# Kernel optimization log

Measured on AMD Instinct MI355X. Metric: run time of the kernel, lower is better.

Reference implementation:

```python
import jax, jax.numpy as jnp
import numpy as np

B, N, D, E, R = 2, 50000, 128, 500000, 500
LN_EPS = 1e-5


def setup_inputs() -> dict:
    key = jax.random.key(0)
    ks = jax.random.split(key, 12)
    s = 1.0 / np.sqrt(D)
    s2 = 1.0 / np.sqrt(2 * D)
    return {
        "h": jax.random.normal(ks[0], (B, N, D), dtype=jnp.float32),
        "edge_src": jax.random.randint(ks[1], (E,), 0, N),
        "edge_tgt": jax.random.randint(ks[2], (E,), 0, N),
        "edge_rel": jax.random.randint(ks[3], (E,), 0, R),
        "nE": N,
        "msg_W": jax.random.uniform(ks[4], (D, D), jnp.float32, -s, s),
        "rel_emb": jax.random.normal(ks[5], (R, D), dtype=jnp.float32),
        "gate_W": jax.random.uniform(ks[6], (D, D), jnp.float32, -s, s),
        "update_W": jax.random.uniform(ks[7], (2 * D, D), jnp.float32, -s2, s2),
        "update_b": jax.random.uniform(ks[8], (D,), jnp.float32, -s2, s2),
        "ln_gamma": jnp.ones((D,), jnp.float32),
        "ln_beta": jnp.zeros((D,), jnp.float32),
    }


def reference(h, edge_src, edge_tgt, edge_rel, nE, msg_W, rel_emb, gate_W,
              update_W, update_b, ln_gamma, ln_beta):
    r = rel_emb[edge_rel]                      # [E, D]
    h_src = h[:, edge_src]                     # [B, E, D] gather
    gate = jax.nn.sigmoid(h_src @ gate_W)      # [B, E, D]
    msg = (h_src @ msg_W) * r[None] * gate     # [B, E, D]
    # scatter_add over target nodes
    h_agg = jnp.zeros((h.shape[0], nE, h.shape[2]), h.dtype)
    h_agg = h_agg.at[:, edge_tgt].add(msg)     # [B, N, D]
    upd = jnp.concatenate([h, h_agg], axis=-1) @ update_W + update_b
    x = h + jax.nn.relu(upd)
    mu = jnp.mean(x, axis=-1, keepdims=True)
    var = jnp.var(x, axis=-1, keepdims=True)
    h_new = (x - mu) * jax.lax.rsqrt(var + LN_EPS) * ln_gamma + ln_beta
    return h_new
```

## Files before the change

### kernel.cpp

```cpp
#include <hip/hip_runtime.h>

#define DD 128
#define NN 50000
#define BB 2
#define EE 500000
#define CAP 64
#define LN_EPS 1e-5f

typedef __attribute__((ext_vector_type(8))) short bf16x8;
typedef __attribute__((ext_vector_type(4))) float f32x4;

union FragU { unsigned short u[8]; unsigned int q[4]; bf16x8 v; };

__device__ __forceinline__ unsigned short f2bf(float x) {
  union { float f; unsigned u; } v; v.f = x;
  unsigned r = (v.u + 0x7FFFu + ((v.u >> 16) & 1u)) >> 16;
  return (unsigned short)r;
}
__device__ __forceinline__ float bfbits(short s) {
  union { unsigned u; float f; } v;
  v.u = ((unsigned)(unsigned short)s) << 16;
  return v.f;
}
__device__ __forceinline__ float sigmoidf(float x) {
  return 1.0f / (1.0f + __expf(-x));
}

__device__ __forceinline__ void stage16(const void* g, void* l) {
  __builtin_amdgcn_global_load_lds(
      (const __attribute__((address_space(1))) unsigned int*)g,
      (__attribute__((address_space(3))) unsigned int*)l, 16, 0, 0);
}

__global__ __launch_bounds__(256) void k_node(
    const float* __restrict__ h, const float* __restrict__ gate_W,
    const float* __restrict__ msg_W, unsigned short* __restrict__ P,
    const float* __restrict__ rel_emb, unsigned short* __restrict__ relb,
    int* __restrict__ deg, int BN)
{
  __shared__ float Hs[3][2048];

  const int t    = threadIdx.x;

  {
    const int gid  = blockIdx.x * 256 + t;
    const int gsz2 = gridDim.x * 256;
    for (int i = gid; i < 500 * 64; i += gsz2) {
      const float a = rel_emb[2 * i];
      const float b = rel_emb[2 * i + 1];
      *(unsigned int*)&relb[2 * i] =
          (unsigned int)f2bf(a) | ((unsigned int)f2bf(b) << 16);
    }
    for (int i = gid; i < NN; i += gsz2) deg[i] = 0;
    asm volatile("s_waitcnt vmcnt(0)" ::: "memory");
    __builtin_amdgcn_sched_barrier(0);
  }

  const int lane = t & 63;
  const int n16  = lane & 15;
  const int quad = lane >> 4;
  const int wave = t >> 6;

  FragU ag[2][4], am[2][4];
#pragma unroll
  for (int fi = 0; fi < 2; fi++) {
    const int frow = (wave + fi * 4) * 16 + n16;
#pragma unroll
    for (int ks = 0; ks < 4; ks++) {
      const int k0 = ks * 32 + quad * 8;
#pragma unroll
      for (int e = 0; e < 8; e++) {
        ag[fi][ks].u[e] = f2bf(gate_W[(size_t)(k0 + e) * DD + frow]);
        am[fi][ks].u[e] = f2bf(msg_W[(size_t)(k0 + e) * DD + frow]);
      }
    }
  }

  const int sr = t >> 5, sc = t & 31;
  const size_t g0 = (size_t)sr * 512 +
                    (size_t)((((sc & 24) | ((sc & 7) ^ (sr & 7)))) << 4);

  const int nT    = BN >> 4;
  const int gstep = gridDim.x;
  const int bid   = blockIdx.x;
  const char* hB  = (const char*)h;

#define NSTAGE(slot, tl)                                                     \
  do {                                                                       \
    const char* gb = hB + ((size_t)(tl) << 13);                              \
    char* lb = (char*)&Hs[slot][0];                                          \
    stage16(gb + g0, lb + t * 16);                                           \
    stage16(gb + g0 + 4096, lb + 4096 + t * 16);                             \
  } while (0)

  if (bid < nT)         NSTAGE(0, bid);
  if (bid + gstep < nT) NSTAGE(1, bid + gstep);

  int s = 0;
  for (int tile = bid; tile < nT; tile += gstep) {
    asm volatile("s_waitcnt vmcnt(2)" ::: "memory");
    __builtin_amdgcn_s_barrier();
    asm volatile("" ::: "memory");
    __builtin_amdgcn_sched_barrier(0);

    const float* hs = &Hs[s][0];
    bf16x8 bfr[4];
#pragma unroll
    for (int ks = 0; ks < 4; ks++) {
      const int cc = ks * 8 + quad * 2;
      const int w0 = (cc & 24) | ((cc & 7) ^ (n16 & 7));
      const int w1 = ((cc + 1) & 24) | (((cc + 1) & 7) ^ (n16 & 7));
      const float4 x0 = *(const float4*)(hs + n16 * 128 + w0 * 4);
      const float4 x1 = *(const float4*)(hs + n16 * 128 + w1 * 4);
      FragU f;
      f.u[0] = f2bf(x0.x); f.u[1] = f2bf(x0.y);
      f.u[2] = f2bf(x0.z); f.u[3] = f2bf(x0.w);
      f.u[4] = f2bf(x1.x); f.u[5] = f2bf(x1.y);
      f.u[6] = f2bf(x1.z); f.u[7] = f2bf(x1.w);
      bfr[ks] = f.v;
    }

    f32x4 accg[2], accm[2];
#pragma unroll
    for (int fi = 0; fi < 2; fi++) { accg[fi] = (f32x4)0.f; accm[fi] = (f32x4)0.f; }

#pragma unroll
    for (int fi = 0; fi < 2; fi++)
#pragma unroll
      for (int ks = 0; ks < 4; ks++) {
        accg[fi] = __builtin_amdgcn_mfma_f32_16x16x32_bf16(ag[fi][ks].v, bfr[ks], accg[fi], 0, 0, 0);
        accm[fi] = __builtin_amdgcn_mfma_f32_16x16x32_bf16(am[fi][ks].v, bfr[ks], accm[fi], 0, 0, 0);
      }

    const int b    = (tile * 16 >= NN) ? 1 : 0;
    const int node = tile * 16 + n16 - b * NN;
    unsigned short* Pr = P + (size_t)node * 256 + b * 128;
#pragma unroll
    for (int fi = 0; fi < 2; fi++) {
      const int ft = wave + fi * 4;
      const float v0 = accm[fi][0] * sigmoidf(accg[fi][0]);
      const float v1 = accm[fi][1] * sigmoidf(accg[fi][1]);
      const float v2 = accm[fi][2] * sigmoidf(accg[fi][2]);
      const float v3 = accm[fi][3] * sigmoidf(accg[fi][3]);
      uint2 o;
      o.x = (unsigned int)f2bf(v0) | ((unsigned int)f2bf(v1) << 16);
      o.y = (unsigned int)f2bf(v2) | ((unsigned int)f2bf(v3) << 16);
      *(uint2*)(Pr + ft * 16 + quad * 4) = o;
    }

    asm volatile("" ::: "memory");
    if (tile + 2 * gstep < nT) {
      int s2 = s + 2; if (s2 >= 3) s2 -= 3;
      NSTAGE(s2, tile + 2 * gstep);
    }
    s = (s + 1 >= 3) ? 0 : s + 1;
  }
#undef NSTAGE
}

__global__ __launch_bounds__(256) void k_fill_direct(
    const int* __restrict__ esrc, const int* __restrict__ etgt,
    const int* __restrict__ erel, int* __restrict__ deg,
    int* __restrict__ packed)
{
  const int e = blockIdx.x * 256 + threadIdx.x;
  if (e < EE) {
    const int tgt = etgt[e];
    const int pos = atomicAdd(&deg[tgt], 1);
    if (pos < CAP) packed[(size_t)tgt * CAP + pos] = esrc[e] | (erel[e] << 16);
  }
}

__global__ __launch_bounds__(256) void k_agg(
    const unsigned short* __restrict__ P, const unsigned short* __restrict__ relb,
    const int* __restrict__ deg, const int* __restrict__ packed,
    unsigned short* __restrict__ h_agg)
{
  const int node = blockIdx.x * 4 + (threadIdx.x >> 6);
  if (node >= NN) return;
  const int lane = threadIdx.x & 63;
  const int half = lane >> 5;
  const int c8   = (lane & 31) * 8;
  const int rc   = c8 & 127;

  const int beg = node * CAP;
  const int cnt = min(deg[node], CAP);
  const int end = beg + cnt;

  float acc[8];
#pragma unroll
  for (int i = 0; i < 8; i++) acc[i] = 0.f;

  int j = beg + half;
  for (; j + 2 < end; j += 4) {
    const int p0 = packed[j];
    const int p1 = packed[j + 2];
    const bf16x8 pv0 = *(const bf16x8*)(P + (size_t)(p0 & 0xFFFF) * 256 + c8);
    const bf16x8 rv0 = *(const bf16x8*)(relb + (size_t)(p0 >> 16) * DD + rc);
    const bf16x8 pv1 = *(const bf16x8*)(P + (size_t)(p1 & 0xFFFF) * 256 + c8);
    const bf16x8 rv1 = *(const bf16x8*)(relb + (size_t)(p1 >> 16) * DD + rc);
#pragma unroll
    for (int i = 0; i < 8; i++) {
      acc[i] += bfbits(pv0[i]) * bfbits(rv0[i]);
      acc[i] += bfbits(pv1[i]) * bfbits(rv1[i]);
    }
  }
  for (; j < end; j += 2) {
    const int p0 = packed[j];
    const bf16x8 pv0 = *(const bf16x8*)(P + (size_t)(p0 & 0xFFFF) * 256 + c8);
    const bf16x8 rv0 = *(const bf16x8*)(relb + (size_t)(p0 >> 16) * DD + rc);
#pragma unroll
    for (int i = 0; i < 8; i++) acc[i] += bfbits(pv0[i]) * bfbits(rv0[i]);
  }

#pragma unroll
  for (int i = 0; i < 8; i++) acc[i] += __shfl_xor(acc[i], 32, 64);

  if (half == 0) {
    uint4 o;
    o.x = (unsigned int)f2bf(acc[0]) | ((unsigned int)f2bf(acc[1]) << 16);
    o.y = (unsigned int)f2bf(acc[2]) | ((unsigned int)f2bf(acc[3]) << 16);
    o.z = (unsigned int)f2bf(acc[4]) | ((unsigned int)f2bf(acc[5]) << 16);
    o.w = (unsigned int)f2bf(acc[6]) | ((unsigned int)f2bf(acc[7]) << 16);
    *(uint4*)(h_agg + (size_t)node * 256 + c8) = o;
  }
}

__global__ __launch_bounds__(256) void k_update_ln(
    const float* __restrict__ h, const unsigned short* __restrict__ h_agg,
    const float* __restrict__ upd_W, const float* __restrict__ upd_b,
    const float* __restrict__ gamma, const float* __restrict__ beta,
    float* __restrict__ out, int BN)
{
  __shared__ float Us[3][3072];
  __shared__ float Rs[4][16], Rq[4][16];

  const int t    = threadIdx.x;
  const int lane = t & 63;
  const int n16  = lane & 15;
  const int quad = lane >> 4;
  const int wave = t >> 6;

  FragU aw[2][8];
#pragma unroll
  for (int fi = 0; fi < 2; fi++) {
    const int frow = (wave + fi * 4) * 16 + n16;
#pragma unroll
    for (int ks = 0; ks < 8; ks++) {
      const int k0 = ks * 32 + quad * 8;
#pragma unroll
      for (int e = 0; e < 8; e++)
        aw[fi][ks].u[e] = f2bf(upd_W[(size_t)(k0 + e) * DD + frow]);
    }
  }

  float4 bv[2], gv[2], btv[2];
#pragma unroll
  for (int fi = 0; fi < 2; fi++) {
    const int f0 = (wave + fi * 4) * 16 + quad * 4;
    bv[fi]  = *(const float4*)(upd_b + f0);
    gv[fi]  = *(const float4*)(gamma + f0);
    btv[fi] = *(const float4*)(beta + f0);
  }

  const int sr = t >> 5, sc = t & 31;
  const size_t g0 = (size_t)sr * 512 +
                    (size_t)((((sc & 24) | ((sc & 7) ^ (sr & 7)))) << 4);
  const int ar = t >> 4, ac = t & 15;
  const size_t ga0 = (size_t)ar * 512 +
                     (size_t)((((ac & 8) | ((ac & 7) ^ (ar & 7)))) << 4);

  const int nT    = BN >> 4;
  const int gstep = gridDim.x;
  const int bid   = blockIdx.x;
  const char* hB  = (const char*)h;
  const char* aB  = (const char*)h_agg;

#define USTAGE(slot, tl)                                                     \
  do {                                                                       \
    const char* gb = hB + ((size_t)(tl) << 13);                              \
    char* lb = (char*)&Us[slot][0];                                          \
    stage16(gb + g0, lb + t * 16);                                           \
    stage16(gb + g0 + 4096, lb + 4096 + t * 16);                             \
    const int bb = ((tl) * 16 >= NN) ? 1 : 0;                                \
    const size_t node0 = (size_t)(tl) * 16 - (size_t)bb * NN;                \
    stage16(aB + (node0 << 9) + ((size_t)bb << 8) + ga0, lb + 8192 + t * 16);\
  } while (0)

  if (bid < nT)         USTAGE(0, bid);
  if (bid + gstep < nT) USTAGE(1, bid + gstep);

  int s = 0;
  for (int tile = bid; tile < nT; tile += gstep) {
    asm volatile("s_waitcnt vmcnt(3)" ::: "memory");
    __builtin_amdgcn_s_barrier();
    asm volatile("" ::: "memory");
    __builtin_amdgcn_sched_barrier(0);

    const float* hs = &Us[s][0];
    const unsigned short* ha = (const unsigned short*)(hs + 2048);

    bf16x8 bfr[8];
#pragma unroll
    for (int ks = 0; ks < 4; ks++) {
      const int cc = ks * 8 + quad * 2;
      const int w0 = (cc & 24) | ((cc & 7) ^ (n16 & 7));
      const int w1 = ((cc + 1) & 24) | (((cc + 1) & 7) ^ (n16 & 7));
      const float4 x0 = *(const float4*)(hs + n16 * 128 + w0 * 4);
      const float4 x1 = *(const float4*)(hs + n16 * 128 + w1 * 4);
      FragU f;
      f.u[0] = f2bf(x0.x); f.u[1] = f2bf(x0.y);
      f.u[2] = f2bf(x0.z); f.u[3] = f2bf(x0.w);
      f.u[4] = f2bf(x1.x); f.u[5] = f2bf(x1.y);
      f.u[6] = f2bf(x1.z); f.u[7] = f2bf(x1.w);
      bfr[ks] = f.v;
    }
#pragma unroll
    for (int ks = 0; ks < 4; ks++) {
      const int c  = ks * 4 + quad;
      const int wc = (c & 8) | ((c & 7) ^ (n16 & 7));
      bfr[4 + ks] = *(const bf16x8*)(ha + n16 * 128 + wc * 8);
    }

    f32x4 acc[2];
#pragma unroll
    for (int fi = 0; fi < 2; fi++) acc[fi] = (f32x4)0.f;
#pragma unroll
    for (int fi = 0; fi < 2; fi++)
#pragma unroll
      for (int ks = 0; ks < 8; ks++)
        acc[fi] = __builtin_amdgcn_mfma_f32_16x16x32_bf16(aw[fi][ks].v, bfr[ks], acc[fi], 0, 0, 0);

    float xv[2][4];
    float p1 = 0.f, p2 = 0.f;
#pragma unroll
    for (int fi = 0; fi < 2; fi++) {
      const int ft = wave + fi * 4;
      const int cr = ft * 4 + quad;
      const int wr = (cr & 24) | ((cr & 7) ^ (n16 & 7));
      const float4 hv = *(const float4*)(hs + n16 * 128 + wr * 4);
      xv[fi][0] = hv.x + fmaxf(acc[fi][0] + bv[fi].x, 0.f);
      xv[fi][1] = hv.y + fmaxf(acc[fi][1] + bv[fi].y, 0.f);
      xv[fi][2] = hv.z + fmaxf(acc[fi][2] + bv[fi].z, 0.f);
      xv[fi][3] = hv.w + fmaxf(acc[fi][3] + bv[fi].w, 0.f);
#pragma unroll
      for (int r = 0; r < 4; r++) { p1 += xv[fi][r]; p2 += xv[fi][r] * xv[fi][r]; }
    }
    p1 += __shfl_xor(p1, 16, 64); p2 += __shfl_xor(p2, 16, 64);
    p1 += __shfl_xor(p1, 32, 64); p2 += __shfl_xor(p2, 32, 64);
    if (quad == 0) { Rs[wave][n16] = p1; Rq[wave][n16] = p2; }
    asm volatile("s_waitcnt lgkmcnt(0)" ::: "memory");
    __builtin_amdgcn_s_barrier();
    asm volatile("" ::: "memory");
    const float sA = Rs[0][n16] + Rs[1][n16] + Rs[2][n16] + Rs[3][n16];
    const float sB = Rq[0][n16] + Rq[1][n16] + Rq[2][n16] + Rq[3][n16];

    const float mu   = sA * (1.0f / DD);
    const float var  = sB * (1.0f / DD) - mu * mu;
    const float rstd = rsqrtf(var + LN_EPS);

    const size_t nrow = (size_t)tile * 16 + n16;
#pragma unroll
    for (int fi = 0; fi < 2; fi++) {
      const int f0 = (wave + fi * 4) * 16 + quad * 4;
      float4 o;
      o.x = (xv[fi][0] - mu) * rstd * gv[fi].x + btv[fi].x;
      o.y = (xv[fi][1] - mu) * rstd * gv[fi].y + btv[fi].y;
      o.z = (xv[fi][2] - mu) * rstd * gv[fi].z + btv[fi].z;
      o.w = (xv[fi][3] - mu) * rstd * gv[fi].w + btv[fi].w;
      *(float4*)(out + nrow * DD + f0) = o;
    }

    asm volatile("" ::: "memory");
    if (tile + 2 * gstep < nT) {
      int s2 = s + 2; if (s2 >= 3) s2 -= 3;
      USTAGE(s2, tile + 2 * gstep);
    }
    s = (s + 1 >= 3) ? 0 : s + 1;
  }
#undef USTAGE
}

extern "C" void kernel_launch(void* const* d_in, const int* in_sizes, int n_in,
                              void* d_out, int out_size, void* d_ws, size_t ws_size,
                              hipStream_t stream) {
  const float* h       = (const float*)d_in[0];
  const int*   esrc    = (const int*)d_in[1];
  const int*   etgt    = (const int*)d_in[2];
  const int*   erel    = (const int*)d_in[3];
  const float* msg_W   = (const float*)d_in[5];
  const float* rel_emb = (const float*)d_in[6];
  const float* gate_W  = (const float*)d_in[7];
  const float* upd_W   = (const float*)d_in[8];
  const float* upd_b   = (const float*)d_in[9];
  const float* gamma   = (const float*)d_in[10];
  const float* beta    = (const float*)d_in[11];
  float*       out     = (float*)d_out;

  const int BN = in_sizes[0] / DD;

  unsigned short* P     = (unsigned short*)d_ws;
  unsigned short* h_agg = P + (size_t)NN * 256;
  unsigned short* relb  = h_agg + (size_t)NN * 256;
  int* deg    = (int*)(relb + 500 * DD);
  int* packed = deg + NN;

  const int nbE = (EE + 255) / 256;

  k_node<<<512, 256, 0, stream>>>(h, gate_W, msg_W, P, rel_emb, relb, deg, BN);

  k_fill_direct<<<nbE, 256, 0, stream>>>(esrc, etgt, erel, deg, packed);

  k_agg<<<(NN + 3) / 4, 256, 0, stream>>>(P, relb, deg, packed, h_agg);

  k_update_ln<<<512, 256, 0, stream>>>(h, h_agg, upd_W, upd_b,
                                       gamma, beta, out, BN);
}
```

Measured before the change: 227.5 us.

## Fuse neighbor aggregation into update+LayerNorm kernel with LDS double buffering

Merges the gather-aggregate kernel into the update/LayerNorm kernel. Each 16-node tile's aggregated messages for both batches are computed directly into LDS, so the bf16 h_agg round trip through global memory and one kernel launch go away. The bf16 relation-embedding conversion is dropped and fp32 rel_emb is read directly. The update kernel now runs on 512 persistent blocks, prefetching the next tile's aggregation while computing the current one. This risks lower parallelism for the latency-bound gather, since it moves from roughly 12.5k blocks to 512, and the synchronous register loads replace async LDS staging.

```diff
diff --git a/kernel.cpp b/kernel.cpp
--- a/kernel.cpp
+++ b/kernel.cpp
@@ -35,7 +35,6 @@
 __global__ __launch_bounds__(256) void k_node(
     const float* __restrict__ h, const float* __restrict__ gate_W,
     const float* __restrict__ msg_W, unsigned short* __restrict__ P,
-    const float* __restrict__ rel_emb, unsigned short* __restrict__ relb,
     int* __restrict__ deg, int BN)
 {
   __shared__ float Hs[3][2048];
@@ -45,12 +44,6 @@
   {
     const int gid  = blockIdx.x * 256 + t;
     const int gsz2 = gridDim.x * 256;
-    for (int i = gid; i < 500 * 64; i += gsz2) {
-      const float a = rel_emb[2 * i];
-      const float b = rel_emb[2 * i + 1];
-      *(unsigned int*)&relb[2 * i] =
-          (unsigned int)f2bf(a) | ((unsigned int)f2bf(b) << 16);
-    }
     for (int i = gid; i < NN; i += gsz2) deg[i] = 0;
     asm volatile("s_waitcnt vmcnt(0)" ::: "memory");
     __builtin_amdgcn_sched_barrier(0);
@@ -171,75 +164,25 @@
   }
 }
 
-__global__ __launch_bounds__(256) void k_agg(
-    const unsigned short* __restrict__ P, const unsigned short* __restrict__ relb,
-    const int* __restrict__ deg, const int* __restrict__ packed,
-    unsigned short* __restrict__ h_agg)
+__global__ __launch_bounds__(256, 2) void k_upd(
+    const float* __restrict__ h, const unsigned short* __restrict__ P,
+    const float* __restrict__ rel_emb, const int* __restrict__ deg,
+    const int* __restrict__ packed, const float* __restrict__ upd_W,
+    const float* __restrict__ upd_b, const float* __restrict__ gamma,
+    const float* __restrict__ beta, float* __restrict__ out)
 {
-  const int node = blockIdx.x * 4 + (threadIdx.x >> 6);
-  if (node >= NN) return;
-  const int lane = threadIdx.x & 63;
-  const int half = lane >> 5;
-  const int c8   = (lane & 31) * 8;
-  const int rc   = c8 & 127;
-
-  const int beg = node * CAP;
-  const int cnt = min(deg[node], CAP);
-  const int end = beg + cnt;
-
-  float acc[8];
-#pragma unroll
-  for (int i = 0; i < 8; i++) acc[i] = 0.f;
-
-  int j = beg + half;
-  for (; j + 2 < end; j += 4) {
-    const int p0 = packed[j];
-    const int p1 = packed[j + 2];
-    const bf16x8 pv0 = *(const bf16x8*)(P + (size_t)(p0 & 0xFFFF) * 256 + c8);
-    const bf16x8 rv0 = *(const bf16x8*)(relb + (size_t)(p0 >> 16) * DD + rc);
-    const bf16x8 pv1 = *(const bf16x8*)(P + (size_t)(p1 & 0xFFFF) * 256 + c8);
-    const bf16x8 rv1 = *(const bf16x8*)(relb + (size_t)(p1 >> 16) * DD + rc);
-#pragma unroll
-    for (int i = 0; i < 8; i++) {
-      acc[i] += bfbits(pv0[i]) * bfbits(rv0[i]);
-      acc[i] += bfbits(pv1[i]) * bfbits(rv1[i]);
-    }
-  }
-  for (; j < end; j += 2) {
-    const int p0 = packed[j];
-    const bf16x8 pv0 = *(const bf16x8*)(P + (size_t)(p0 & 0xFFFF) * 256 + c8);
-    const bf16x8 rv0 = *(const bf16x8*)(relb + (size_t)(p0 >> 16) * DD + rc);
-#pragma unroll
-    for (int i = 0; i < 8; i++) acc[i] += bfbits(pv0[i]) * bfbits(rv0[i]);
-  }
-
-#pragma unroll
-  for (int i = 0; i < 8; i++) acc[i] += __shfl_xor(acc[i], 32, 64);
-
-  if (half == 0) {
-    uint4 o;
-    o.x = (unsigned int)f2bf(acc[0]) | ((unsigned int)f2bf(acc[1]) << 16);
-    o.y = (unsigned int)f2bf(acc[2]) | ((unsigned int)f2bf(acc[3]) << 16);
-    o.z = (unsigned int)f2bf(acc[4]) | ((unsigned int)f2bf(acc[5]) << 16);
-    o.w = (unsigned int)f2bf(acc[6]) | ((unsigned int)f2bf(acc[7]) << 16);
-    *(uint4*)(h_agg + (size_t)node * 256 + c8) = o;
-  }
-}
-
-__global__ __launch_bounds__(256) void k_update_ln(
-    const float* __restrict__ h, const unsigned short* __restrict__ h_agg,
-    const float* __restrict__ upd_W, const float* __restrict__ upd_b,
-    const float* __restrict__ gamma, const float* __restrict__ beta,
-    float* __restrict__ out, int BN)
-{
-  __shared__ float Us[3][3072];
-  __shared__ float Rs[4][16], Rq[4][16];
+  __shared__ unsigned short Ab[2][16 * 256];
+  __shared__ float Hb[2][2 * 2048];
+  __shared__ float Rs[2][4][16], Rq[2][4][16];
 
   const int t    = threadIdx.x;
   const int lane = t & 63;
   const int n16  = lane & 15;
   const int quad = lane >> 4;
   const int wave = t >> 6;
+  const int half = lane >> 5;
+  const int c8   = (lane & 31) * 8;
+  const int rc   = c8 & 127;
 
   FragU aw[2][8];
 #pragma unroll
@@ -263,122 +206,175 @@
     btv[fi] = *(const float4*)(beta + f0);
   }
 
-  const int sr = t >> 5, sc = t & 31;
-  const size_t g0 = (size_t)sr * 512 +
-                    (size_t)((((sc & 24) | ((sc & 7) ^ (sr & 7)))) << 4);
-  const int ar = t >> 4, ac = t & 15;
-  const size_t ga0 = (size_t)ar * 512 +
-                     (size_t)((((ac & 8) | ((ac & 7) ^ (ar & 7)))) << 4);
-
-  const int nT    = BN >> 4;
+  const int sr  = t >> 5, sc = t & 31;
+  const int scw  = (sc & 24) | ((sc & 7) ^ (sr & 7));
+  const int scw2 = (sc & 24) | ((sc & 7) ^ ((sr + 8) & 7));
+
+  const int nTL   = NN / 16;
   const int gstep = gridDim.x;
   const int bid   = blockIdx.x;
-  const char* hB  = (const char*)h;
-  const char* aB  = (const char*)h_agg;
-
-#define USTAGE(slot, tl)                                                     \
-  do {                                                                       \
-    const char* gb = hB + ((size_t)(tl) << 13);                              \
-    char* lb = (char*)&Us[slot][0];                                          \
-    stage16(gb + g0, lb + t * 16);                                           \
-    stage16(gb + g0 + 4096, lb + 4096 + t * 16);                             \
-    const int bb = ((tl) * 16 >= NN) ? 1 : 0;                                \
-    const size_t node0 = (size_t)(tl) * 16 - (size_t)bb * NN;                \
-    stage16(aB + (node0 << 9) + ((size_t)bb << 8) + ga0, lb + 8192 + t * 16);\
+
+#define STAGE(buf, stl)                                                       \
+  do {                                                                        \
+    const size_t r0 = (size_t)(stl) * 16;                                     \
+    const float4 ha0 = *(const float4*)(h + (r0 + sr) * DD + sc * 4);         \
+    const float4 ha1 = *(const float4*)(h + (r0 + sr + 8) * DD + sc * 4);     \
+    const float4 hb0 = *(const float4*)(h + (r0 + NN + sr) * DD + sc * 4);    \
+    const float4 hb1 = *(const float4*)(h + (r0 + NN + sr + 8) * DD + sc * 4);\
+    for (int rr = 0; rr < 4; rr++) {                                          \
+      const int r = wave * 4 + rr;                                            \
+      const int n = (stl) * 16 + r;                                           \
+      const int beg = n * CAP;                                                \
+      const int dg  = deg[n];                                                 \
+      const int end = beg + (dg < CAP ? dg : CAP);                            \
+      float acc[8];                                                           \
+      _Pragma("unroll")                                                       \
+      for (int i = 0; i < 8; i++) acc[i] = 0.f;                               \
+      int j = beg + half;                                                     \
+      for (; j + 2 < end; j += 4) {                                           \
+        const int p0 = packed[j];                                             \
+        const int p1 = packed[j + 2];                                         \
+        const bf16x8 pv0 = *(const bf16x8*)(P + (size_t)(p0 & 0xFFFF) * 256 + c8); \
+        const float4 ra0 = *(const float4*)(rel_emb + (size_t)(p0 >> 16) * DD + rc); \
+        const float4 rb0 = *(const float4*)(rel_emb + (size_t)(p0 >> 16) * DD + rc + 4); \
+        const bf16x8 pv1 = *(const bf16x8*)(P + (size_t)(p1 & 0xFFFF) * 256 + c8); \
+        const float4 ra1 = *(const float4*)(rel_emb + (size_t)(p1 >> 16) * DD + rc); \
+        const float4 rb1 = *(const float4*)(rel_emb + (size_t)(p1 >> 16) * DD + rc + 4); \
+        acc[0] += bfbits(pv0[0]) * ra0.x;  acc[0] += bfbits(pv1[0]) * ra1.x;  \
+        acc[1] += bfbits(pv0[1]) * ra0.y;  acc[1] += bfbits(pv1[1]) * ra1.y;  \
+        acc[2] += bfbits(pv0[2]) * ra0.z;  acc[2] += bfbits(pv1[2]) * ra1.z;  \
+        acc[3] += bfbits(pv0[3]) * ra0.w;  acc[3] += bfbits(pv1[3]) * ra1.w;  \
+        acc[4] += bfbits(pv0[4]) * rb0.x;  acc[4] += bfbits(pv1[4]) * rb1.x;  \
+        acc[5] += bfbits(pv0[5]) * rb0.y;  acc[5] += bfbits(pv1[5]) * rb1.y;  \
+        acc[6] += bfbits(pv0[6]) * rb0.z;  acc[6] += bfbits(pv1[6]) * rb1.z;  \
+        acc[7] += bfbits(pv0[7]) * rb0.w;  acc[7] += bfbits(pv1[7]) * rb1.w;  \
+      }                                                                       \
+      for (; j < end; j += 2) {                                               \
+        const int p0 = packed[j];                                             \
+        const bf16x8 pv0 = *(const bf16x8*)(P + (size_t)(p0 & 0xFFFF) * 256 + c8); \
+        const float4 ra0 = *(const float4*)(rel_emb + (size_t)(p0 >> 16) * DD + rc); \
+        const float4 rb0 = *(const float4*)(rel_emb + (size_t)(p0 >> 16) * DD + rc + 4); \
+        acc[0] += bfbits(pv0[0]) * ra0.x;                                     \
+        acc[1] += bfbits(pv0[1]) * ra0.y;                                     \
+        acc[2] += bfbits(pv0[2]) * ra0.z;                                     \
+        acc[3] += bfbits(pv0[3]) * ra0.w;                                     \
+        acc[4] += bfbits(pv0[4]) * rb0.x;                                     \
+        acc[5] += bfbits(pv0[5]) * rb0.y;                                     \
+        acc[6] += bfbits(pv0[6]) * rb0.z;                                     \
+        acc[7] += bfbits(pv0[7]) * rb0.w;                                     \
+      }                                                                       \
+      _Pragma("unroll")                                                       \
+      for (int i = 0; i < 8; i++) acc[i] += __shfl_xor(acc[i], 32, 64);       \
+      if (half == 0) {                                                        \
+        uint4 o;                                                              \
+        o.x = (unsigned int)f2bf(acc[0]) | ((unsigned int)f2bf(acc[1]) << 16);\
+        o.y = (unsigned int)f2bf(acc[2]) | ((unsigned int)f2bf(acc[3]) << 16);\
+        o.z = (unsigned int)f2bf(acc[4]) | ((unsigned int)f2bf(acc[5]) << 16);\
+        o.w = (unsigned int)f2bf(acc[6]) | ((unsigned int)f2bf(acc[7]) << 16);\
+        const int g   = lane;                                                 \
+        const int gsw = (g & 24) | ((g & 7) ^ (r & 7));                       \
+        *(uint4*)&Ab[buf][r * 256 + gsw * 8] = o;                             \
+      }                                                                       \
+    }                                                                         \
+    *(float4*)&Hb[buf][0 * 2048 + sr * 128 + scw * 4]        = ha0;           \
+    *(float4*)&Hb[buf][0 * 2048 + (sr + 8) * 128 + scw2 * 4] = ha1;           \
+    *(float4*)&Hb[buf][1 * 2048 + sr * 128 + scw * 4]        = hb0;           \
+    *(float4*)&Hb[buf][1 * 2048 + (sr + 8) * 128 + scw2 * 4] = hb1;           \
   } while (0)
 
-  if (bid < nT)         USTAGE(0, bid);
-  if (bid + gstep < nT) USTAGE(1, bid + gstep);
-
-  int s = 0;
-  for (int tile = bid; tile < nT; tile += gstep) {
-    asm volatile("s_waitcnt vmcnt(3)" ::: "memory");
-    __builtin_amdgcn_s_barrier();
-    asm volatile("" ::: "memory");
-    __builtin_amdgcn_sched_barrier(0);
-
-    const float* hs = &Us[s][0];
-    const unsigned short* ha = (const unsigned short*)(hs + 2048);
-
-    bf16x8 bfr[8];
-#pragma unroll
-    for (int ks = 0; ks < 4; ks++) {
-      const int cc = ks * 8 + quad * 2;
-      const int w0 = (cc & 24) | ((cc & 7) ^ (n16 & 7));
-      const int w1 = ((cc + 1) & 24) | (((cc + 1) & 7) ^ (n16 & 7));
-      const float4 x0 = *(const float4*)(hs + n16 * 128 + w0 * 4);
-      const float4 x1 = *(const float4*)(hs + n16 * 128 + w1 * 4);
-      FragU f;
-      f.u[0] = f2bf(x0.x); f.u[1] = f2bf(x0.y);
-      f.u[2] = f2bf(x0.z); f.u[3] = f2bf(x0.w);
-      f.u[4] = f2bf(x1.x); f.u[5] = f2bf(x1.y);
-      f.u[6] = f2bf(x1.z); f.u[7] = f2bf(x1.w);
-      bfr[ks] = f.v;
-    }
-#pragma unroll
-    for (int ks = 0; ks < 4; ks++) {
-      const int c  = ks * 4 + quad;
-      const int wc = (c & 8) | ((c & 7) ^ (n16 & 7));
-      bfr[4 + ks] = *(const bf16x8*)(ha + n16 * 128 + wc * 8);
-    }
-
-    f32x4 acc[2];
-#pragma unroll
-    for (int fi = 0; fi < 2; fi++) acc[fi] = (f32x4)0.f;
-#pragma unroll
-    for (int fi = 0; fi < 2; fi++)
-#pragma unroll
-      for (int ks = 0; ks < 8; ks++)
-        acc[fi] = __builtin_amdgcn_mfma_f32_16x16x32_bf16(aw[fi][ks].v, bfr[ks], acc[fi], 0, 0, 0);
-
-    float xv[2][4];
-    float p1 = 0.f, p2 = 0.f;
-#pragma unroll
-    for (int fi = 0; fi < 2; fi++) {
-      const int ft = wave + fi * 4;
-      const int cr = ft * 4 + quad;
-      const int wr = (cr & 24) | ((cr & 7) ^ (n16 & 7));
-      const float4 hv = *(const float4*)(hs + n16 * 128 + wr * 4);
-      xv[fi][0] = hv.x + fmaxf(acc[fi][0] + bv[fi].x, 0.f);
-      xv[fi][1] = hv.y + fmaxf(acc[fi][1] + bv[fi].y, 0.f);
-      xv[fi][2] = hv.z + fmaxf(acc[fi][2] + bv[fi].z, 0.f);
-      xv[fi][3] = hv.w + fmaxf(acc[fi][3] + bv[fi].w, 0.f);
-#pragma unroll
-      for (int r = 0; r < 4; r++) { p1 += xv[fi][r]; p2 += xv[fi][r] * xv[fi][r]; }
-    }
-    p1 += __shfl_xor(p1, 16, 64); p2 += __shfl_xor(p2, 16, 64);
-    p1 += __shfl_xor(p1, 32, 64); p2 += __shfl_xor(p2, 32, 64);
-    if (quad == 0) { Rs[wave][n16] = p1; Rq[wave][n16] = p2; }
+  if (bid < nTL) STAGE(0, bid);
+  asm volatile("s_waitcnt lgkmcnt(0)" ::: "memory");
+  __builtin_amdgcn_s_barrier();
+  asm volatile("" ::: "memory");
+
+  int cur = 0;
+  for (int tl = bid; tl < nTL; tl += gstep) {
+    const int ntl = tl + gstep;
+    if (ntl < nTL) STAGE(cur ^ 1, ntl);
+
+#pragma unroll
+    for (int tau = 0; tau < 2; tau++) {
+      const float* hs = &Hb[cur][tau * 2048];
+      const unsigned short* ab = &Ab[cur][0];
+
+      bf16x8 bfr[8];
+#pragma unroll
+      for (int ks = 0; ks < 4; ks++) {
+        const int cc = ks * 8 + quad * 2;
+        const int w0 = (cc & 24) | ((cc & 7) ^ (n16 & 7));
+        const int w1 = ((cc + 1) & 24) | (((cc + 1) & 7) ^ (n16 & 7));
+        const float4 x0 = *(const float4*)(hs + n16 * 128 + w0 * 4);
+        const float4 x1 = *(const float4*)(hs + n16 * 128 + w1 * 4);
+        FragU f;
+        f.u[0] = f2bf(x0.x); f.u[1] = f2bf(x0.y);
+        f.u[2] = f2bf(x0.z); f.u[3] = f2bf(x0.w);
+        f.u[4] = f2bf(x1.x); f.u[5] = f2bf(x1.y);
+        f.u[6] = f2bf(x1.z); f.u[7] = f2bf(x1.w);
+        bfr[ks] = f.v;
+      }
+#pragma unroll
+      for (int ks = 0; ks < 4; ks++) {
+        const int g   = tau * 16 + ks * 4 + quad;
+        const int gsw = (g & 24) | ((g & 7) ^ (n16 & 7));
+        bfr[4 + ks] = *(const bf16x8*)(ab + n16 * 256 + gsw * 8);
+      }
+
+      f32x4 acc2[2];
+#pragma unroll
+      for (int fi = 0; fi < 2; fi++) acc2[fi] = (f32x4)0.f;
+#pragma unroll
+      for (int fi = 0; fi < 2; fi++)
+#pragma unroll
+        for (int ks = 0; ks < 8; ks++)
+          acc2[fi] = __builtin_amdgcn_mfma_f32_16x16x32_bf16(aw[fi][ks].v, bfr[ks], acc2[fi], 0, 0, 0);
+
+      float xv[2][4];
+      float p1 = 0.f, p2 = 0.f;
+#pragma unroll
+      for (int fi = 0; fi < 2; fi++) {
+        const int ft = wave + fi * 4;
+        const int cr = ft * 4 + quad;
+        const int wr = (cr & 24) | ((cr & 7) ^ (n16 & 7));
+        const float4 hv = *(const float4*)(hs + n16 * 128 + wr * 4);
+        xv[fi][0] = hv.x + fmaxf(acc2[fi][0] + bv[fi].x, 0.f);
+        xv[fi][1] = hv.y + fmaxf(acc2[fi][1] + bv[fi].y, 0.f);
+        xv[fi][2] = hv.z + fmaxf(acc2[fi][2] + bv[fi].z, 0.f);
+        xv[fi][3] = hv.w + fmaxf(acc2[fi][3] + bv[fi].w, 0.f);
+#pragma unroll
+        for (int r = 0; r < 4; r++) { p1 += xv[fi][r]; p2 += xv[fi][r] * xv[fi][r]; }
+      }
+      p1 += __shfl_xor(p1, 16, 64); p2 += __shfl_xor(p2, 16, 64);
+      p1 += __shfl_xor(p1, 32, 64); p2 += __shfl_xor(p2, 32, 64);
+      if (quad == 0) { Rs[tau][wave][n16] = p1; Rq[tau][wave][n16] = p2; }
+      asm volatile("s_waitcnt lgkmcnt(0)" ::: "memory");
+      __builtin_amdgcn_s_barrier();
+      asm volatile("" ::: "memory");
+      const float sA = Rs[tau][0][n16] + Rs[tau][1][n16] + Rs[tau][2][n16] + Rs[tau][3][n16];
+      const float sB = Rq[tau][0][n16] + Rq[tau][1][n16] + Rq[tau][2][n16] + Rq[tau][3][n16];
+
+      const float mu   = sA * (1.0f / DD);
+      const float var  = sB * (1.0f / DD) - mu * mu;
+      const float rstd = rsqrtf(var + LN_EPS);
+
+      const size_t nrow = (size_t)tau * NN + (size_t)tl * 16 + n16;
+#pragma unroll
+      for (int fi = 0; fi < 2; fi++) {
+        const int f0 = (wave + fi * 4) * 16 + quad * 4;
+        float4 o;
+        o.x = (xv[fi][0] - mu) * rstd * gv[fi].x + btv[fi].x;
+        o.y = (xv[fi][1] - mu) * rstd * gv[fi].y + btv[fi].y;
+        o.z = (xv[fi][2] - mu) * rstd * gv[fi].z + btv[fi].z;
+        o.w = (xv[fi][3] - mu) * rstd * gv[fi].w + btv[fi].w;
+        *(float4*)(out + nrow * DD + f0) = o;
+      }
+    }
+
     asm volatile("s_waitcnt lgkmcnt(0)" ::: "memory");
     __builtin_amdgcn_s_barrier();
     asm volatile("" ::: "memory");
-    const float sA = Rs[0][n16] + Rs[1][n16] + Rs[2][n16] + Rs[3][n16];
-    const float sB = Rq[0][n16] + Rq[1][n16] + Rq[2][n16] + Rq[3][n16];
-
-    const float mu   = sA * (1.0f / DD);
-    const float var  = sB * (1.0f / DD) - mu * mu;
-    const float rstd = rsqrtf(var + LN_EPS);
-
-    const size_t nrow = (size_t)tile * 16 + n16;
-#pragma unroll
-    for (int fi = 0; fi < 2; fi++) {
-      const int f0 = (wave + fi * 4) * 16 + quad * 4;
-      float4 o;
-      o.x = (xv[fi][0] - mu) * rstd * gv[fi].x + btv[fi].x;
-      o.y = (xv[fi][1] - mu) * rstd * gv[fi].y + btv[fi].y;
-      o.z = (xv[fi][2] - mu) * rstd * gv[fi].z + btv[fi].z;
-      o.w = (xv[fi][3] - mu) * rstd * gv[fi].w + btv[fi].w;
-      *(float4*)(out + nrow * DD + f0) = o;
-    }
-
-    asm volatile("" ::: "memory");
-    if (tile + 2 * gstep < nT) {
-      int s2 = s + 2; if (s2 >= 3) s2 -= 3;
-      USTAGE(s2, tile + 2 * gstep);
-    }
-    s = (s + 1 >= 3) ? 0 : s + 1;
-  }
-#undef USTAGE
+    cur ^= 1;
+  }
+#undef STAGE
 }
 
 extern "C" void kernel_launch(void* const* d_in, const int* in_sizes, int n_in,
@@ -399,20 +395,16 @@
 
   const int BN = in_sizes[0] / DD;
 
-  unsigned short* P     = (unsigned short*)d_ws;
-  unsigned short* h_agg = P + (size_t)NN * 256;
-  unsigned short* relb  = h_agg + (size_t)NN * 256;
-  int* deg    = (int*)(relb + 500 * DD);
+  unsigned short* P = (unsigned short*)d_ws;
+  int* deg    = (int*)(P + (size_t)NN * 256);
   int* packed = deg + NN;
 
   const int nbE = (EE + 255) / 256;
 
-  k_node<<<512, 256, 0, stream>>>(h, gate_W, msg_W, P, rel_emb, relb, deg, BN);
+  k_node<<<512, 256, 0, stream>>>(h, gate_W, msg_W, P, deg, BN);
 
   k_fill_direct<<<nbE, 256, 0, stream>>>(esrc, etgt, erel, deg, packed);
 
-  k_agg<<<(NN + 3) / 4, 256, 0, stream>>>(P, relb, deg, packed, h_agg);
-
-  k_update_ln<<<512, 256, 0, stream>>>(h, h_agg, upd_W, upd_b,
-                                       gamma, beta, out, BN);
-}
+  k_upd<<<512, 256, 0, stream>>>(h, P, rel_emb, deg, packed, upd_W, upd_b,
+                                 gamma, beta, out);
+}
```

New measurement: 267.1 us. +17.4%, slower.
